# Performance work log

Hardware: AMD Instinct MI355X
Metric: run time of the kernel (lower is better)

Reference implementation:

```python
import jax, jax.numpy as jnp
import numpy as np

N, E, IN, HID, OUT = 50000, 800000, 128, 64, 32
ALPHA, BETA, DIVIDER = 0.5, 0.5, 5.0


def _gcn_conv(x, edge_index, W, b, alpha=ALPHA, beta=BETA):
    """DirectedGCNConv.forward: add self loops, linear, degree-normalized gather-mul-scatter."""
    n = x.shape[0]
    loops = jnp.arange(n, dtype=edge_index.dtype)
    row = jnp.concatenate([edge_index[0], loops])  # sources
    col = jnp.concatenate([edge_index[1], loops])  # targets
    x = x @ W.T + b                                # [n, out]
    ones = jnp.ones(row.shape[0], dtype=x.dtype)
    in_deg = jax.ops.segment_sum(ones, col, num_segments=n)
    out_deg = jax.ops.segment_sum(ones, row, num_segments=n)
    norm = in_deg[col] ** (-alpha) * out_deg[row] ** (-beta)  # [E+n]
    msgs = norm[:, None] * x[row]                  # gather + scale
    return jax.ops.segment_sum(msgs, col, num_segments=n)  # scatter-add aggr


def _source_enc(x, ei, W1, b1, W2, b2):
    x = jax.nn.relu(_gcn_conv(x, ei, W1, b1))
    return _gcn_conv(x, jnp.flip(ei, axis=0), W2, b2)


def _target_enc(x, ei, W1, b1, W2, b2):
    x = jax.nn.relu(_gcn_conv(x, jnp.flip(ei, axis=0), W1, b1))
    return _gcn_conv(x, ei, W2, b2)


def setup_inputs() -> dict:
    key = jax.random.key(0)
    ks = jax.random.split(key, 24)

    def lin(kw, kb, o, i, scale):
        return (jax.random.normal(kw, (o, i), jnp.float32) * scale,
                jax.random.normal(kb, (o,), jnp.float32) * 0.01)

    s1 = (2.0 / (IN + HID)) ** 0.5
    s2 = (2.0 / (HID + OUT)) ** 0.5
    inp = {
        "s": jax.random.normal(ks[0], (N, IN), jnp.float32),
        "t": jax.random.normal(ks[1], (N, IN), jnp.float32),
        "edge_index": jax.random.randint(ks[2], (2, E), 0, N, jnp.int32),
        "noise_s": jax.random.normal(ks[3], (N, OUT), jnp.float32),
        "noise_t": jax.random.normal(ks[4], (N, OUT), jnp.float32),
    }
    names = ["sm", "sl", "tm", "tl"]  # source/target mu/logstd encoders
    k = 5
    for nm in names:
        W1, b1 = lin(ks[k], ks[k + 1], HID, IN, s1); k += 2
        W2, b2 = lin(ks[k], ks[k + 1], OUT, HID, s2); k += 2
        inp[nm + "1_W"], inp[nm + "1_b"] = W1, b1
        inp[nm + "2_W"], inp[nm + "2_b"] = W2, b2
    return inp


def reference(s, t, edge_index, noise_s, noise_t,
              sm1_W, sm1_b, sm2_W, sm2_b,
              sl1_W, sl1_b, sl2_W, sl2_b,
              tm1_W, tm1_b, tm2_W, tm2_b,
              tl1_W, tl1_b, tl2_W, tl2_b):
    s_mu = _source_enc(s, edge_index, sm1_W, sm1_b, sm2_W, sm2_b)
    s_logstd = _source_enc(s, edge_index, sl1_W, sl1_b, sl2_W, sl2_b)
    t_mu = _target_enc(t, edge_index, tm1_W, tm1_b, tm2_W, tm2_b)
    t_logstd = _target_enc(t, edge_index, tl1_W, tl1_b, tl2_W, tl2_b)
    # reparametrize_edges (training mode), noise materialized as input
    s_out = s_mu + noise_s * jnp.exp(s_logstd) / DIVIDER
    t_out = t_mu + noise_t * jnp.exp(t_logstd) / DIVIDER
    return (s_out, t_out)
```

## Files before the change

kernel.cpp:

```cpp
#include <hip/hip_runtime.h>
#include <hip/hip_fp16.h>
#include <math.h>

#define N_NODES 50000
#define NPACK 25000
#define E_EDGES 800000
#define NCHUNKS ((N_NODES + 1023) / 1024)
#define LIN_BLOCKS 1564
#define QCH 64
#define CHUNK (E_EDGES / QCH)
#define CHUNK4 (CHUNK / 4)
#define OCT_NODES 6250
#define OCT_PACK 3125
#define HF_BLOCKS 1024
#define HL_GRID (HF_BLOCKS + LIN_BLOCKS)
#define LCAP 2048

typedef _Float16 half8 __attribute__((ext_vector_type(8)));
typedef float f32x4 __attribute__((ext_vector_type(4)));

__device__ inline float fac_from(unsigned int u) {
    unsigned short us = (unsigned short)(u >> 16);
    __half h;
    __builtin_memcpy(&h, &us, 2);
    return __half2float(h);
}

__device__ inline int unpack_cnt(const unsigned int* cntp, int i) {
    unsigned int w = cntp[i >> 1];
    return (i & 1) ? (int)(w >> 16) : (int)(w & 0xffff);
}

__global__ __launch_bounds__(256) void hist_lin1_kernel(const int* __restrict__ ei0,
                                                        const int* __restrict__ ei1,
                                                        unsigned int* __restrict__ ghist,
                                                        unsigned short* __restrict__ list,
                                                        unsigned int* __restrict__ cnt_bkt,
                                                        const float* __restrict__ Xs,
                                                        const float* __restrict__ Xt,
                                                        const float* __restrict__ sWa,
                                                        const float* __restrict__ sba,
                                                        const float* __restrict__ sWb,
                                                        const float* __restrict__ sbb,
                                                        const float* __restrict__ tWa,
                                                        const float* __restrict__ tba,
                                                        const float* __restrict__ tWb,
                                                        const float* __restrict__ tbb,
                                                        __half* __restrict__ As,
                                                        __half* __restrict__ At, int n) {
    __shared__ unsigned int h[OCT_PACK];
    __shared__ unsigned int lcnt;
    int bx = blockIdx.x;
    int tid = threadIdx.x;
    if (bx < HF_BLOCKS) {
        int oct = bx & 7, q = (bx >> 3) & 63, dir = bx >> 9;
        for (int i = tid; i < OCT_PACK; i += 256) h[i] = 0;
        if (tid == 0) lcnt = 0;
        __syncthreads();
        const int* key = dir ? ei0 : ei1;
        const uint4* key4 = (const uint4*)(key + q * CHUNK);
        unsigned short* lst = list + ((size_t)(dir * QCH + q) * 8 + oct) * LCAP;
        int lo = oct * OCT_NODES;
        int lane = tid & 63;
        for (int j = tid; j < CHUNK4; j += 256) {
            uint4 k4 = key4[j];
            int vv[4] = { (int)k4.x, (int)k4.y, (int)k4.z, (int)k4.w };
#pragma unroll
            for (int e = 0; e < 4; ++e) {
                unsigned int d = (unsigned int)(vv[e] - lo);
                bool pred = d < OCT_NODES;
                if (pred) atomicAdd(&h[d >> 1], 1u << ((d & 1) * 16));
                unsigned long long m = __ballot(pred);
                if (m) {
                    int pre = __popcll(m & ((1ull << lane) - 1));
                    int tot = __popcll(m);
                    int ldr = __ffsll((unsigned long long)m) - 1;
                    unsigned int base = 0;
                    if (lane == ldr) base = atomicAdd(&lcnt, (unsigned int)tot);
                    base = __shfl(base, ldr);
                    unsigned int slot = base + (unsigned int)pre;
                    if (pred && slot < LCAP) lst[slot] = (unsigned short)(j * 4 + e);
                }
            }
        }
        __syncthreads();
        unsigned int* g = ghist + (size_t)(dir * QCH + q) * NPACK + oct * OCT_PACK;
        for (int i = tid; i < OCT_PACK; i += 256) g[i] = h[i];
        if (tid == 0) cnt_bkt[dir * 512 + q * 8 + oct] = (lcnt < LCAP) ? lcnt : LCAP;
        return;
    }
    int lidx = bx - HF_BLOCKS;
    int y = lidx & 1;
    int xb = lidx >> 1;
    const float* X = y ? Xt : Xs;
    const float* Wset[2] = { y ? tWa : sWa, y ? tWb : sWb };
    const float* bset[2] = { y ? tba : sba, y ? tbb : sbb };
    __half* A = y ? At : As;

    int w = tid >> 6, lane = tid & 63;
    int quad = lane >> 4, col = lane & 15;
    int node0 = xb * 64 + w * 16;

    half8 afrag[4];
    {
        int row = node0 + col;
        if (row >= n) row = n - 1;
        const float* xr = X + (size_t)row * 128 + quad * 8;
#pragma unroll
        for (int kc = 0; kc < 4; ++kc) {
            float4 f0 = *(const float4*)(xr + kc * 32);
            float4 f1 = *(const float4*)(xr + kc * 32 + 4);
            half8 hh;
            hh[0] = (_Float16)f0.x; hh[1] = (_Float16)f0.y;
            hh[2] = (_Float16)f0.z; hh[3] = (_Float16)f0.w;
            hh[4] = (_Float16)f1.x; hh[5] = (_Float16)f1.y;
            hh[6] = (_Float16)f1.z; hh[7] = (_Float16)f1.w;
            afrag[kc] = hh;
        }
    }

#pragma unroll
    for (int set = 0; set < 2; ++set) {
        const float* Ws = Wset[set];
#pragma unroll
        for (int nt = 0; nt < 4; ++nt) {
            float bb = bset[set][nt * 16 + col];
            f32x4 acc = { bb, bb, bb, bb };
            const float* wr = Ws + (size_t)(nt * 16 + col) * 128 + quad * 8;
#pragma unroll
            for (int kc = 0; kc < 4; ++kc) {
                float4 f0 = *(const float4*)(wr + kc * 32);
                float4 f1 = *(const float4*)(wr + kc * 32 + 4);
                half8 bfr;
                bfr[0] = (_Float16)f0.x; bfr[1] = (_Float16)f0.y;
                bfr[2] = (_Float16)f0.z; bfr[3] = (_Float16)f0.w;
                bfr[4] = (_Float16)f1.x; bfr[5] = (_Float16)f1.y;
                bfr[6] = (_Float16)f1.z; bfr[7] = (_Float16)f1.w;
                acc = __builtin_amdgcn_mfma_f32_16x16x32_f16(afrag[kc], bfr, acc, 0, 0, 0);
            }
#pragma unroll
            for (int r = 0; r < 4; ++r) {
                int node = node0 + quad * 4 + r;
                if (node < n)
                    A[(size_t)node * 128 + set * 64 + nt * 16 + col] = __float2half(acc[r]);
            }
        }
    }
}

__global__ __launch_bounds__(256) void nodescan_kernel(unsigned int* __restrict__ ghist,
                                                       unsigned int* __restrict__ cntp) {
    int vp = blockIdx.x * 256 + threadIdx.x;
    int dir = blockIdx.y;
    if (vp >= NPACK) return;
    unsigned int lo = 0, hi = 0;
    unsigned int* g = ghist + (size_t)dir * QCH * NPACK + vp;
#pragma unroll 4
    for (int q = 0; q < QCH; ++q) {
        unsigned int w = g[(size_t)q * NPACK];
        g[(size_t)q * NPACK] = lo | (hi << 16);
        lo += w & 0xffff;
        hi += w >> 16;
    }
    cntp[dir * NPACK + vp] = lo | (hi << 16);
}

__global__ __launch_bounds__(1024) void scan_chunk2_kernel(const unsigned int* __restrict__ cntp,
                                                           int* __restrict__ offs_f,
                                                           int* __restrict__ offs_b,
                                                           int* __restrict__ part_f,
                                                           int* __restrict__ part_b, int n) {
    const unsigned int* cnt = cntp + (blockIdx.y ? NPACK : 0);
    int* offs = blockIdx.y ? offs_b : offs_f;
    int* partials = blockIdx.y ? part_b : part_f;
    __shared__ int sh[1024];
    int tid = threadIdx.x;
    int i = blockIdx.x * 1024 + tid;
    int v = (i < n) ? unpack_cnt(cnt, i) : 0;
    sh[tid] = v;
    __syncthreads();
    for (int off = 1; off < 1024; off <<= 1) {
        int add = (tid >= off) ? sh[tid - off] : 0;
        __syncthreads();
        sh[tid] += add;
        __syncthreads();
    }
    if (i < n) offs[i] = sh[tid] - v;
    if (tid == 1023) partials[blockIdx.x] = sh[tid];
}

__global__ __launch_bounds__(64) void scan_partials2_kernel(int* part_f, int* part_b, int nchunks) {
    int* p = blockIdx.x ? part_b : part_f;
    __shared__ int sh[64];
    int tid = threadIdx.x;
    int v = (tid < nchunks) ? p[tid] : 0;
    sh[tid] = v;
    __syncthreads();
    for (int off = 1; off < 64; off <<= 1) {
        int add = (tid >= off) ? sh[tid - off] : 0;
        __syncthreads();
        sh[tid] += add;
        __syncthreads();
    }
    if (tid < nchunks) p[tid] = sh[tid] - v;
    if (tid == 63) p[nchunks] = sh[63];
}

__global__ __launch_bounds__(256) void addback_deg_kernel(int* __restrict__ offs_f,
                                                          int* __restrict__ offs_b,
                                                          const int* __restrict__ part_f,
                                                          const int* __restrict__ part_b,
                                                          const unsigned int* __restrict__ cntp,
                                                          float* dsi, float* dti,
                                                          unsigned short* __restrict__ h_dsi,
                                                          unsigned short* __restrict__ h_dti,
                                                          int n, int nchunks) {
    int i = blockIdx.x * 256 + threadIdx.x;
    if (blockIdx.y == 0) {
        if (i < n) {
            offs_f[i] += part_f[i >> 10];
            float f = rsqrtf((float)(unpack_cnt(cntp, i) + 1));
            dti[i] = f;
            __half hf = __float2half(f);
            unsigned short hb; __builtin_memcpy(&hb, &hf, 2);
            h_dti[i] = hb;
        } else if (i == n) offs_f[n] = part_f[nchunks];
    } else {
        if (i < n) {
            offs_b[i] += part_b[i >> 10];
            float f = rsqrtf((float)(unpack_cnt(cntp + NPACK, i) + 1));
            dsi[i] = f;
            __half hf = __float2half(f);
            unsigned short hb; __builtin_memcpy(&hb, &hf, 2);
            h_dsi[i] = hb;
        } else if (i == n) offs_b[n] = part_b[nchunks];
    }
}

__global__ __launch_bounds__(256) void fill_kernel(const int* __restrict__ ei0,
                                                   const int* __restrict__ ei1,
                                                   const unsigned int* __restrict__ ghist,
                                                   const int* __restrict__ offs_f,
                                                   const int* __restrict__ offs_b,
                                                   const unsigned short* __restrict__ h_dsi,
                                                   const unsigned short* __restrict__ h_dti,
                                                   unsigned int* __restrict__ pay_f,
                                                   unsigned int* __restrict__ pay_b,
                                                   const unsigned short* __restrict__ list,
                                                   const unsigned int* __restrict__ cnt_bkt) {
    __shared__ unsigned int pos[OCT_NODES];
    int bx = blockIdx.x;
    int oct = bx & 7, q = (bx >> 3) & 63, dir = bx >> 9;
    int tid = threadIdx.x;
    const unsigned int* pref = ghist + (size_t)(dir * QCH + q) * NPACK + oct * OCT_PACK;
    const int* offs = dir ? offs_b : offs_f;
    int lo = oct * OCT_NODES;
    for (int d = tid; d < OCT_NODES; d += 256) {
        unsigned int pw = pref[d >> 1];
        int cb = (d & 1) ? (int)(pw >> 16) : (int)(pw & 0xffff);
        pos[d] = (unsigned int)(offs[lo + d] + cb);
    }
    __syncthreads();
    const int* key = dir ? ei0 : ei1;
    const int* pid = dir ? ei1 : ei0;
    const unsigned short* hfac = dir ? h_dti : h_dsi;
    unsigned int* pay = dir ? pay_b : pay_f;
    const unsigned short* lst = list + ((size_t)(dir * QCH + q) * 8 + oct) * LCAP;
    int cnt = (int)cnt_bkt[dir * 512 + q * 8 + oct];
    int base = q * CHUNK;
    for (int j = tid; j < cnt; j += 256) {
        int gi = base + (int)lst[j];
        int v = key[gi];
        int id = pid[gi];
        unsigned int p = atomicAdd(&pos[v - lo], 1u);
        unsigned int hb = hfac[id];
        pay[p] = (unsigned int)id | (hb << 16);
    }
}

__device__ inline void acc_fma(float* acc, uint4 u, float f) {
    const __half2* h = (const __half2*)&u;
    float2 f0 = __half22float2(h[0]);
    float2 f1 = __half22float2(h[1]);
    float2 f2 = __half22float2(h[2]);
    float2 f3 = __half22float2(h[3]);
    acc[0] += f * f0.x; acc[1] += f * f0.y; acc[2] += f * f1.x; acc[3] += f * f1.y;
    acc[4] += f * f2.x; acc[5] += f * f2.y; acc[6] += f * f3.x; acc[7] += f * f3.y;
}

__global__ __launch_bounds__(256) void pull_lin2_kernel(const __half* __restrict__ As,
                                                        const __half* __restrict__ At,
                                                        __half* __restrict__ Cs,
                                                        __half* __restrict__ Ct,
                                                        const int* __restrict__ offs_f,
                                                        const int* __restrict__ offs_b,
                                                        const unsigned int* __restrict__ pay_f,
                                                        const unsigned int* __restrict__ pay_b,
                                                        const float* __restrict__ dsi,
                                                        const float* __restrict__ dti,
                                                        const float* __restrict__ sW2a,
                                                        const float* __restrict__ sb2a,
                                                        const float* __restrict__ sW2b,
                                                        const float* __restrict__ sb2b,
                                                        const float* __restrict__ tW2a,
                                                        const float* __restrict__ tb2a,
                                                        const float* __restrict__ tW2b,
                                                        const float* __restrict__ tb2b, int n) {
    int y = blockIdx.y;
    const __half* xw = y ? At : As;
    __half* C = y ? Ct : Cs;
    const int* offs = y ? offs_b : offs_f;
    const unsigned int* pay = y ? pay_b : pay_f;
    const float* fac_self  = y ? dsi : dti;
    const float* fac_other = y ? dti : dsi;
    const float* W2a = y ? tW2a : sW2a;  const float* b2a = y ? tb2a : sb2a;
    const float* W2b = y ? tW2b : sW2b;  const float* b2b = y ? tb2b : sb2b;

    __shared__ float Wt[64 * 66];
    __shared__ float bsh[64];
    __shared__ float xs[16 * 132];

    int tid = threadIdx.x;
    for (int idx = tid; idx < 2048; idx += 256) {
        int o = idx >> 6, k = idx & 63;
        Wt[k * 66 + o]      = W2a[idx];
        Wt[k * 66 + 33 + o] = W2b[idx];
    }
    if (tid < 32) { bsh[tid] = b2a[tid]; bsh[32 + tid] = b2b[tid]; }

    int ln = tid >> 4;
    int f4 = tid & 15;
    int v = blockIdx.x * 16 + ln;
    int i = offs[v], end = offs[v + 1];
    const uint4* xw16 = (const uint4*)xw;

    float acc[8] = {0, 0, 0, 0, 0, 0, 0, 0};
    acc_fma(acc, xw16[v * 16 + f4], fac_other[v]);
    while (i < end && (i & 3)) {
        unsigned int pk = pay[i];
        acc_fma(acc, xw16[(pk & 0xffff) * 16 + f4], fac_from(pk));
        ++i;
    }
    for (; i + 3 < end; i += 4) {
        uint4 pk = *(const uint4*)(pay + i);
        int s0 = pk.x & 0xffff, s1 = pk.y & 0xffff;
        int s2 = pk.z & 0xffff, s3 = pk.w & 0xffff;
        uint4 ua = xw16[s0 * 16 + f4];
        uint4 ub = xw16[s1 * 16 + f4];
        uint4 uc = xw16[s2 * 16 + f4];
        uint4 ud = xw16[s3 * 16 + f4];
        acc_fma(acc, ua, fac_from(pk.x));
        acc_fma(acc, ub, fac_from(pk.y));
        acc_fma(acc, uc, fac_from(pk.z));
        acc_fma(acc, ud, fac_from(pk.w));
    }
    for (; i < end; ++i) {
        unsigned int pk = pay[i];
        acc_fma(acc, xw16[(pk & 0xffff) * 16 + f4], fac_from(pk));
    }

    float fs = fac_self[v];
    float4 a0, a1;
    a0.x = fmaxf(acc[0] * fs, 0.0f); a0.y = fmaxf(acc[1] * fs, 0.0f);
    a0.z = fmaxf(acc[2] * fs, 0.0f); a0.w = fmaxf(acc[3] * fs, 0.0f);
    a1.x = fmaxf(acc[4] * fs, 0.0f); a1.y = fmaxf(acc[5] * fs, 0.0f);
    a1.z = fmaxf(acc[6] * fs, 0.0f); a1.w = fmaxf(acc[7] * fs, 0.0f);
    *(float4*)&xs[ln * 132 + f4 * 8]     = a0;
    *(float4*)&xs[ln * 132 + f4 * 8 + 4] = a1;
    __syncthreads();

    int nn = tid >> 5, o = tid & 31;
    const float* x0 = &xs[nn * 132];
    const float* x1 = &xs[(nn + 8) * 132];
    float am0 = bsh[o], al0 = bsh[32 + o];
    float am1 = am0,    al1 = al0;
#pragma unroll 4
    for (int k = 0; k < 64; ++k) {
        float wm = Wt[k * 66 + o], wl = Wt[k * 66 + 33 + o];
        am0 += x0[k] * wm;  al0 += x0[64 + k] * wl;
        am1 += x1[k] * wm;  al1 += x1[64 + k] * wl;
    }
    int v0 = blockIdx.x * 16 + nn;
    int v1 = v0 + 8;
    C[v0 * 64 + o]      = __float2half(am0);
    C[v0 * 64 + 32 + o] = __float2half(al0);
    C[v1 * 64 + o]      = __float2half(am1);
    C[v1 * 64 + 32 + o] = __float2half(al1);
}

__global__ __launch_bounds__(256) void final_pull2_kernel(const __half* __restrict__ Cs,
                                                          const __half* __restrict__ Ct,
                                                          float* __restrict__ out_s,
                                                          float* __restrict__ out_t,
                                                          const int* __restrict__ offs_f,
                                                          const int* __restrict__ offs_b,
                                                          const unsigned int* __restrict__ pay_f,
                                                          const unsigned int* __restrict__ pay_b,
                                                          const float* __restrict__ dsi,
                                                          const float* __restrict__ dti,
                                                          const float* __restrict__ noise_s,
                                                          const float* __restrict__ noise_t,
                                                          int n) {
    int y = blockIdx.y;
    const __half* xw = y ? Ct : Cs;
    float* out = y ? out_t : out_s;
    const int* offs = y ? offs_f : offs_b;
    const unsigned int* pay = y ? pay_f : pay_b;
    const float* fac_self  = y ? dti : dsi;
    const float* fac_other = y ? dsi : dti;
    const float* noise = y ? noise_t : noise_s;

    const uint4* xw16 = (const uint4*)xw;
    int ln = threadIdx.x >> 3;
    int f4 = threadIdx.x & 7;
    int v = blockIdx.x * 32 + ln;
    if (v >= n) return;
    int i = offs[v], end = offs[v + 1];

    float acc[8] = {0, 0, 0, 0, 0, 0, 0, 0};
    acc_fma(acc, xw16[v * 8 + f4], fac_other[v]);
    while (i < end && (i & 3)) {
        unsigned int pk = pay[i];
        acc_fma(acc, xw16[(pk & 0xffff) * 8 + f4], fac_from(pk));
        ++i;
    }
    for (; i + 3 < end; i += 4) {
        uint4 pk = *(const uint4*)(pay + i);
        int s0 = pk.x & 0xffff, s1 = pk.y & 0xffff;
        int s2 = pk.z & 0xffff, s3 = pk.w & 0xffff;
        uint4 ua = xw16[s0 * 8 + f4];
        uint4 ub = xw16[s1 * 8 + f4];
        uint4 uc = xw16[s2 * 8 + f4];
        uint4 ud = xw16[s3 * 8 + f4];
        acc_fma(acc, ua, fac_from(pk.x));
        acc_fma(acc, ub, fac_from(pk.y));
        acc_fma(acc, uc, fac_from(pk.z));
        acc_fma(acc, ud, fac_from(pk.w));
    }
    for (; i < end; ++i) {
        unsigned int pk = pay[i];
        acc_fma(acc, xw16[(pk & 0xffff) * 8 + f4], fac_from(pk));
    }

    float fs = fac_self[v];
#pragma unroll
    for (int j = 0; j < 8; ++j) acc[j] *= fs;

    int lane = threadIdx.x & 63;
    float lg[8];
#pragma unroll
    for (int j = 0; j < 8; ++j) lg[j] = __shfl(acc[j], lane + 4);
    if (f4 < 4) {
        const float4* nz4 = (const float4*)noise;
        float4 n0 = nz4[v * 8 + f4 * 2];
        float4 n1 = nz4[v * 8 + f4 * 2 + 1];
        float4 r0, r1;
        r0.x = acc[0] + n0.x * expf(lg[0]) * 0.2f;
        r0.y = acc[1] + n0.y * expf(lg[1]) * 0.2f;
        r0.z = acc[2] + n0.z * expf(lg[2]) * 0.2f;
        r0.w = acc[3] + n0.w * expf(lg[3]) * 0.2f;
        r1.x = acc[4] + n1.x * expf(lg[4]) * 0.2f;
        r1.y = acc[5] + n1.y * expf(lg[5]) * 0.2f;
        r1.z = acc[6] + n1.z * expf(lg[6]) * 0.2f;
        r1.w = acc[7] + n1.w * expf(lg[7]) * 0.2f;
        float4* o4 = (float4*)out;
        o4[v * 8 + f4 * 2]     = r0;
        o4[v * 8 + f4 * 2 + 1] = r1;
    }
}

extern "C" void kernel_launch(void* const* d_in, const int* in_sizes, int n_in,
                              void* d_out, int out_size, void* d_ws, size_t ws_size,
                              hipStream_t stream) {
    const float* s       = (const float*)d_in[0];
    const float* t       = (const float*)d_in[1];
    const int*   ei      = (const int*)d_in[2];
    const float* noise_s = (const float*)d_in[3];
    const float* noise_t = (const float*)d_in[4];
    const float* sm1_W = (const float*)d_in[5];  const float* sm1_b = (const float*)d_in[6];
    const float* sm2_W = (const float*)d_in[7];  const float* sm2_b = (const float*)d_in[8];
    const float* sl1_W = (const float*)d_in[9];  const float* sl1_b = (const float*)d_in[10];
    const float* sl2_W = (const float*)d_in[11]; const float* sl2_b = (const float*)d_in[12];
    const float* tm1_W = (const float*)d_in[13]; const float* tm1_b = (const float*)d_in[14];
    const float* tm2_W = (const float*)d_in[15]; const float* tm2_b = (const float*)d_in[16];
    const float* tl1_W = (const float*)d_in[17]; const float* tl1_b = (const float*)d_in[18];
    const float* tl2_W = (const float*)d_in[19]; const float* tl2_b = (const float*)d_in[20];

    const int* ei0 = ei;
    const int* ei1 = ei + E_EDGES;

    __half* A_s = (__half*)d_ws;
    __half* A_t = A_s + (size_t)N_NODES * 128;
    __half* C_s = A_t + (size_t)N_NODES * 128;
    __half* C_t = C_s + (size_t)N_NODES * 64;
    unsigned int* pay_fwd = (unsigned int*)(C_t + (size_t)N_NODES * 64);
    unsigned int* pay_bwd = pay_fwd + E_EDGES;
    float* dsi = (float*)(pay_bwd + E_EDGES);
    float* dti = dsi + N_NODES;
    int* offs_fwd = (int*)(dti + N_NODES);
    int* offs_bwd = offs_fwd + N_NODES + 1;
    unsigned int* cntp = (unsigned int*)(offs_bwd + N_NODES + 1);
    int* part_fwd = (int*)(cntp + 2 * NPACK);
    int* part_bwd = part_fwd + NCHUNKS + 1;
    unsigned short* h_dsi = (unsigned short*)(part_bwd + NCHUNKS + 1);
    unsigned short* h_dti = h_dsi + N_NODES;
    unsigned short* list  = h_dti + N_NODES;
    unsigned int* cnt_bkt = (unsigned int*)(list + (size_t)HF_BLOCKS * LCAP);

    unsigned int* ghist = (unsigned int*)C_s;

    float* s_out = (float*)d_out;
    float* t_out = (float*)d_out + N_NODES * 32;

    dim3 blk(256);
    dim3 agrid((N_NODES + 1 + 255) / 256, 2);
    dim3 pgrid(N_NODES / 16, 2);
    dim3 fgrid((N_NODES + 31) / 32, 2);
    dim3 nsgrid((NPACK + 255) / 256, 2);

    hist_lin1_kernel<<<HL_GRID, blk, 0, stream>>>(
        ei0, ei1, ghist, list, cnt_bkt,
        s, t, sm1_W, sm1_b, sl1_W, sl1_b, tm1_W, tm1_b, tl1_W, tl1_b,
        A_s, A_t, N_NODES);
    nodescan_kernel<<<nsgrid, blk, 0, stream>>>(ghist, cntp);
    scan_chunk2_kernel<<<dim3(NCHUNKS, 2), 1024, 0, stream>>>(
        cntp, offs_fwd, offs_bwd, part_fwd, part_bwd, N_NODES);
    scan_partials2_kernel<<<2, 64, 0, stream>>>(part_fwd, part_bwd, NCHUNKS);
    addback_deg_kernel<<<agrid, blk, 0, stream>>>(offs_fwd, offs_bwd, part_fwd, part_bwd,
                                                  cntp, dsi, dti, h_dsi, h_dti,
                                                  N_NODES, NCHUNKS);
    fill_kernel<<<HF_BLOCKS, blk, 0, stream>>>(ei0, ei1, ghist, offs_fwd, offs_bwd,
                                               h_dsi, h_dti, pay_fwd, pay_bwd,
                                               list, cnt_bkt);

    pull_lin2_kernel<<<pgrid, blk, 0, stream>>>(A_s, A_t, C_s, C_t,
                                                offs_fwd, offs_bwd, pay_fwd, pay_bwd,
                                                dsi, dti,
                                                sm2_W, sm2_b, sl2_W, sl2_b,
                                                tm2_W, tm2_b, tl2_W, tl2_b, N_NODES);
    final_pull2_kernel<<<fgrid, blk, 0, stream>>>(C_s, C_t, s_out, t_out,
                                                  offs_fwd, offs_bwd, pay_fwd, pay_bwd,
                                                  dsi, dti, noise_s, noise_t, N_NODES);
}
```

Baseline: 337.1 us.

## Use MFMA fp16 for second-layer linear in pull kernel with prepacked half weights

Replaces the per-block fp32 shared-memory staging of the 64x32 second-layer weights and the scalar FMA matmul with a 16x16x32 fp16 MFMA. The weights are converted once per call to fp16 by a small new kernel, and the aggregated activations are stored in shared memory as fp16. This removes the per-block weight transpose load into LDS and the scalar inner loop. In exchange it adds a kernel launch and lowers the precision of the activations and weights fed to the matmul.

```diff
diff --git a/kernel.cpp b/kernel.cpp
--- a/kernel.cpp
+++ b/kernel.cpp
@@ -29,6 +29,17 @@
 __device__ inline int unpack_cnt(const unsigned int* cntp, int i) {
     unsigned int w = cntp[i >> 1];
     return (i & 1) ? (int)(w >> 16) : (int)(w & 0xffff);
+}
+
+__global__ __launch_bounds__(256) void w2h_kernel(const float* __restrict__ sW2a,
+                                                  const float* __restrict__ sW2b,
+                                                  const float* __restrict__ tW2a,
+                                                  const float* __restrict__ tW2b,
+                                                  __half* __restrict__ hw2) {
+    int i = blockIdx.x * 256 + threadIdx.x;
+    if (i >= 4 * 2048) return;
+    const float* src[4] = { sW2a, sW2b, tW2a, tW2b };
+    hw2[i] = __float2half(src[i >> 11][i & 2047]);
 }
 
 __global__ __launch_bounds__(256) void hist_lin1_kernel(const int* __restrict__ ei0,
@@ -298,14 +309,11 @@
                                                         const unsigned int* __restrict__ pay_b,
                                                         const float* __restrict__ dsi,
                                                         const float* __restrict__ dti,
-                                                        const float* __restrict__ sW2a,
                                                         const float* __restrict__ sb2a,
-                                                        const float* __restrict__ sW2b,
                                                         const float* __restrict__ sb2b,
-                                                        const float* __restrict__ tW2a,
                                                         const float* __restrict__ tb2a,
-                                                        const float* __restrict__ tW2b,
-                                                        const float* __restrict__ tb2b, int n) {
+                                                        const float* __restrict__ tb2b,
+                                                        const __half* __restrict__ hw2, int n) {
     int y = blockIdx.y;
     const __half* xw = y ? At : As;
     __half* C = y ? Ct : Cs;
@@ -313,21 +321,12 @@
     const unsigned int* pay = y ? pay_b : pay_f;
     const float* fac_self  = y ? dsi : dti;
     const float* fac_other = y ? dti : dsi;
-    const float* W2a = y ? tW2a : sW2a;  const float* b2a = y ? tb2a : sb2a;
-    const float* W2b = y ? tW2b : sW2b;  const float* b2b = y ? tb2b : sb2b;
-
-    __shared__ float Wt[64 * 66];
-    __shared__ float bsh[64];
-    __shared__ float xs[16 * 132];
+    const float* b2a = y ? tb2a : sb2a;
+    const float* b2b = y ? tb2b : sb2b;
+
+    __shared__ __half xsh[16 * 136];
 
     int tid = threadIdx.x;
-    for (int idx = tid; idx < 2048; idx += 256) {
-        int o = idx >> 6, k = idx & 63;
-        Wt[k * 66 + o]      = W2a[idx];
-        Wt[k * 66 + 33 + o] = W2b[idx];
-    }
-    if (tid < 32) { bsh[tid] = b2a[tid]; bsh[32 + tid] = b2b[tid]; }
-
     int ln = tid >> 4;
     int f4 = tid & 15;
     int v = blockIdx.x * 16 + ln;
@@ -360,32 +359,29 @@
     }
 
     float fs = fac_self[v];
-    float4 a0, a1;
-    a0.x = fmaxf(acc[0] * fs, 0.0f); a0.y = fmaxf(acc[1] * fs, 0.0f);
-    a0.z = fmaxf(acc[2] * fs, 0.0f); a0.w = fmaxf(acc[3] * fs, 0.0f);
-    a1.x = fmaxf(acc[4] * fs, 0.0f); a1.y = fmaxf(acc[5] * fs, 0.0f);
-    a1.z = fmaxf(acc[6] * fs, 0.0f); a1.w = fmaxf(acc[7] * fs, 0.0f);
-    *(float4*)&xs[ln * 132 + f4 * 8]     = a0;
-    *(float4*)&xs[ln * 132 + f4 * 8 + 4] = a1;
+    half8 hx;
+#pragma unroll
+    for (int j = 0; j < 8; ++j) hx[j] = (_Float16)fmaxf(acc[j] * fs, 0.0f);
+    *(half8*)&xsh[ln * 136 + f4 * 8] = hx;
     __syncthreads();
 
-    int nn = tid >> 5, o = tid & 31;
-    const float* x0 = &xs[nn * 132];
-    const float* x1 = &xs[(nn + 8) * 132];
-    float am0 = bsh[o], al0 = bsh[32 + o];
-    float am1 = am0,    al1 = al0;
-#pragma unroll 4
-    for (int k = 0; k < 64; ++k) {
-        float wm = Wt[k * 66 + o], wl = Wt[k * 66 + 33 + o];
-        am0 += x0[k] * wm;  al0 += x0[64 + k] * wl;
-        am1 += x1[k] * wm;  al1 += x1[64 + k] * wl;
-    }
-    int v0 = blockIdx.x * 16 + nn;
-    int v1 = v0 + 8;
-    C[v0 * 64 + o]      = __float2half(am0);
-    C[v0 * 64 + 32 + o] = __float2half(al0);
-    C[v1 * 64 + o]      = __float2half(am1);
-    C[v1 * 64 + 32 + o] = __float2half(al1);
+    int w = tid >> 6, lane = tid & 63;
+    int s = w >> 1, nt = w & 1;
+    int quad = lane >> 4, col = lane & 15;
+    float bb = (s ? b2b : b2a)[nt * 16 + col];
+    f32x4 cacc = { bb, bb, bb, bb };
+    const __half* hw = hw2 + (size_t)(y * 2 + s) * 2048;
+#pragma unroll
+    for (int t = 0; t < 2; ++t) {
+        half8 af = *(const half8*)&xsh[col * 136 + s * 64 + t * 32 + quad * 8];
+        half8 bf = *(const half8*)&hw[(nt * 16 + col) * 64 + t * 32 + quad * 8];
+        cacc = __builtin_amdgcn_mfma_f32_16x16x32_f16(af, bf, cacc, 0, 0, 0);
+    }
+    int vbase = blockIdx.x * 16 + quad * 4;
+    int o = s * 32 + nt * 16 + col;
+#pragma unroll
+    for (int r = 0; r < 4; ++r)
+        C[(size_t)(vbase + r) * 64 + o] = __float2half(cacc[r]);
 }
 
 __global__ __launch_bounds__(256) void final_pull2_kernel(const __half* __restrict__ Cs,
@@ -506,6 +502,7 @@
     unsigned short* h_dti = h_dsi + N_NODES;
     unsigned short* list  = h_dti + N_NODES;
     unsigned int* cnt_bkt = (unsigned int*)(list + (size_t)HF_BLOCKS * LCAP);
+    __half* hw2 = (__half*)(((uintptr_t)(cnt_bkt + 1024) + 15) & ~(uintptr_t)15);
 
     unsigned int* ghist = (unsigned int*)C_s;
 
@@ -518,6 +515,7 @@
     dim3 fgrid((N_NODES + 31) / 32, 2);
     dim3 nsgrid((NPACK + 255) / 256, 2);
 
+    w2h_kernel<<<32, blk, 0, stream>>>(sm2_W, sl2_W, tm2_W, tl2_W, hw2);
     hist_lin1_kernel<<<HL_GRID, blk, 0, stream>>>(
         ei0, ei1, ghist, list, cnt_bkt,
         s, t, sm1_W, sm1_b, sl1_W, sl1_b, tm1_W, tm1_b, tl1_W, tl1_b,
@@ -536,8 +534,7 @@
     pull_lin2_kernel<<<pgrid, blk, 0, stream>>>(A_s, A_t, C_s, C_t,
                                                 offs_fwd, offs_bwd, pay_fwd, pay_bwd,
                                                 dsi, dti,
-                                                sm2_W, sm2_b, sl2_W, sl2_b,
-                                                tm2_W, tm2_b, tl2_W, tl2_b, N_NODES);
+                                                sm2_b, sl2_b, tm2_b, tl2_b, hw2, N_NODES);
     final_pull2_kernel<<<fgrid, blk, 0, stream>>>(C_s, C_t, s_out, t_out,
                                                   offs_fwd, offs_bwd, pay_fwd, pay_bwd,
                                                   dsi, dti, noise_s, noise_t, N_NODES);
```

After: 321.5 us. -4.6%, faster.
